# Kernel optimization log

Hardware: AMD Instinct MI355X
Metric: run time of the kernel (lower is better)

The kernel has to match this reference:

```python
import jax, jax.numpy as jnp
import numpy as np

N, T = 32, 1024
CIN, H, O, F2 = 64, 128, 16, 16  # F2 = 2 * FiLMed_layers
EPS = 1e-5
SLOPE = 0.01  # nn.LeakyReLU default


def _leaky(x):
    return jnp.where(x >= 0, x, SLOPE * x)


def _ln(x, gamma, beta):
    # x: (N,T,O,H); gamma,beta: (O,H) -> broadcast per channel
    mu = jnp.mean(x, axis=-1, keepdims=True)
    var = jnp.mean(jnp.square(x - mu), axis=-1, keepdims=True)
    return (x - mu) * jax.lax.rsqrt(var + EPS) * gamma + beta


def setup_inputs() -> dict:
    key = jax.random.key(0)
    ks = jax.random.split(key, 7)
    s0 = 1.0 / np.sqrt(CIN)
    s1 = 1.0 / np.sqrt(H)
    return {
        "x": jax.random.normal(ks[0], (N, T, CIN), jnp.float32),
        "W0": jax.random.uniform(ks[1], (O, H, CIN), jnp.float32, -s0, s0),
        "b0": jax.random.uniform(ks[2], (O, H), jnp.float32, -s0, s0),
        "g0": jnp.ones((O, H), jnp.float32),
        "be0": jnp.zeros((O, H), jnp.float32),
        "W1": jax.random.uniform(ks[3], (O, H, H), jnp.float32, -s1, s1),
        "b1": jax.random.uniform(ks[4], (O, H), jnp.float32, -s1, s1),
        "g1": jnp.ones((O, H), jnp.float32),
        "be1": jnp.zeros((O, H), jnp.float32),
        "W2": jax.random.uniform(ks[5], (O, F2, H), jnp.float32, -s1, s1),
        "b2": jax.random.uniform(ks[6], (O, F2), jnp.float32, -s1, s1),
    }


def reference(x, W0, b0, g0, be0, W1, b1, g1, be1, W2, b2):
    # Per-channel MLP, vectorized over the O channel axis.
    h = jnp.einsum("ntc,ohc->ntoh", x, W0) + b0          # (N,T,O,H)
    h = _ln(_leaky(h), g0, be0)
    h = jnp.einsum("ntoh,ogh->ntog", h, W1) + b1         # (N,T,O,H)
    h = _ln(_leaky(h), g1, be1)
    out = jnp.einsum("ntoh,ofh->ntof", h, W2) + b2       # (N,T,O,F2)
    out = _leaky(out)
    # torch: stack(dim=1) -> (N,O,T,F2); moveaxis(1,-1) -> (N,T,F2,O)
    return jnp.moveaxis(out, 2, 3)
```

## Files before the change

### kernel.cpp

```cpp
#include <hip/hip_runtime.h>
#include <hip/hip_bf16.h>

#define NTOK  32768
#define CIN   64
#define HDIM  128
#define O_CH  16
#define F2    16
#define SLOPE 0.01f
#define EPS   1e-5f

#define SW0_STRIDE 72
#define SW1_STRIDE 136
#define SW2_STRIDE 136
#define SH_STRIDE  136
#define SW0_OFF 0
#define SW1_OFF 9216
#define SW2_OFF (9216 + 17408)
#define WIMG_SHORTS 28800
#define SH_OFF  28800
#define SH_ROWS 256
#define SBIAS_OFF (SH_OFF + SH_ROWS * SH_STRIDE)
#define SBIAS_FLOATS 272
#define SGB_OFF (SBIAS_OFF + SBIAS_FLOATS * 2)
#define SGB_FLOATS 512
#define SMEM_SHORTS (SGB_OFF + SGB_FLOATS * 2)

typedef __attribute__((ext_vector_type(8))) short bf16x8;
typedef __attribute__((ext_vector_type(4))) short bf16x4;
typedef __attribute__((ext_vector_type(4))) float f32x4;

__device__ __forceinline__ unsigned short f2b(float f) {
  union { float f; unsigned int i; } v;
  v.f = f;
  unsigned int i = v.i;
  unsigned int r = (i + 0x7fffu + ((i >> 16) & 1u)) >> 16;
  return (unsigned short)r;
}
__device__ __forceinline__ short f2bn(float f) {
  union { __hip_bfloat16 h; short s; } v;
  v.h = __float2bfloat16(f);
  return v.s;
}
__device__ __forceinline__ float leaky(float t) {
  return fmaxf(t, SLOPE * t);
}
__device__ __forceinline__ bf16x8 cvt8(const float* __restrict__ p) {
  float4 a = *(const float4*)p;
  float4 b = *(const float4*)(p + 4);
  bf16x8 r;
  r[0] = (short)f2b(a.x); r[1] = (short)f2b(a.y);
  r[2] = (short)f2b(a.z); r[3] = (short)f2b(a.w);
  r[4] = (short)f2b(b.x); r[5] = (short)f2b(b.y);
  r[6] = (short)f2b(b.z); r[7] = (short)f2b(b.w);
  return r;
}
__device__ __forceinline__ bf16x8 cvt8s(const float* __restrict__ p,
                                        const float* __restrict__ s) {
  bf16x8 r;
#pragma unroll
  for (int i = 0; i < 8; ++i) r[i] = (short)f2b(p[i] * s[i]);
  return r;
}

__device__ __forceinline__ void leaky_ln_store(
    f32x4* acc, unsigned short* __restrict__ sh,
    int row0, int lo16, int quad) {
  float a0 = 0.f, a1 = 0.f, a2 = 0.f, a3 = 0.f;
  float c0 = 0.f, c1 = 0.f, c2 = 0.f, c3 = 0.f;
#pragma unroll
  for (int nt = 0; nt < 8; ++nt) {
    float t0 = leaky(acc[nt][0]);
    float t1 = leaky(acc[nt][1]);
    float t2 = leaky(acc[nt][2]);
    float t3 = leaky(acc[nt][3]);
    acc[nt][0] = t0; acc[nt][1] = t1; acc[nt][2] = t2; acc[nt][3] = t3;
    a0 += t0; a1 += t1; a2 += t2; a3 += t3;
    c0 = fmaf(t0, t0, c0); c1 = fmaf(t1, t1, c1);
    c2 = fmaf(t2, t2, c2); c3 = fmaf(t3, t3, c3);
  }
  float s1 = (a0 + a1) + (a2 + a3);
  float s2 = (c0 + c1) + (c2 + c3);
  s1 += __shfl_xor(s1, 16); s2 += __shfl_xor(s2, 16);
  s1 += __shfl_xor(s1, 32); s2 += __shfl_xor(s2, 32);
  float mu = s1 * (1.0f / 128.0f);
  float var = s2 * (1.0f / 128.0f) - mu * mu;
  float rs = rsqrtf(var + EPS);
  float nm = -mu * rs;
  unsigned short* dst = sh + (row0 + lo16) * SH_STRIDE + quad * 4;
#pragma unroll
  for (int nt = 0; nt < 8; ++nt) {
    bf16x4 p;
    p[0] = f2bn(fmaf(acc[nt][0], rs, nm));
    p[1] = f2bn(fmaf(acc[nt][1], rs, nm));
    p[2] = f2bn(fmaf(acc[nt][2], rs, nm));
    p[3] = f2bn(fmaf(acc[nt][3], rs, nm));
    *(bf16x4*)(dst + nt * 16) = p;
  }
}

__global__ __launch_bounds__(1024)
__attribute__((amdgpu_waves_per_eu(4, 4))) void film_main(
    const float* __restrict__ x,
    const float* __restrict__ W0, const float* __restrict__ b0,
    const float* __restrict__ g0, const float* __restrict__ be0,
    const float* __restrict__ W1, const float* __restrict__ b1,
    const float* __restrict__ g1, const float* __restrict__ be1,
    const float* __restrict__ W2, const float* __restrict__ b2,
    float* __restrict__ out) {
  __shared__ unsigned short smem[SMEM_SHORTS];
  const int tid = threadIdx.x;
  const int c   = blockIdx.x & 7;
  const int o   = (blockIdx.x >> 3) & 15;
  const int q   = blockIdx.x >> 7;
  const int tok0 = (q * 8 + c) * 1024;

  float* sbias = (float*)&smem[SBIAS_OFF];
  float* sgb   = (float*)&smem[SGB_OFF];
  float* sg0v  = sgb;
  float* sbe0v = sgb + 128;
  float* sg1v  = sgb + 256;
  float* sbe1v = sgb + 384;

  if (tid < 128)      sg0v [tid]       = g0 [o * HDIM + tid];
  else if (tid < 256) sbe0v[tid - 128] = be0[o * HDIM + (tid - 128)];
  else if (tid < 384) sg1v [tid - 256] = g1 [o * HDIM + (tid - 256)];
  else if (tid < 512) sbe1v[tid - 384] = be1[o * HDIM + (tid - 384)];
  __syncthreads();

  const float* w0 = W0 + (size_t)o * HDIM * CIN;
  const float* w1 = W1 + (size_t)o * HDIM * HDIM;
  const float* w2 = W2 + (size_t)o * F2 * HDIM;
  {
    int cc = tid, n = cc >> 3, k8 = cc & 7;
    *(bf16x8*)&smem[SW0_OFF + n * SW0_STRIDE + k8 * 8] = cvt8(w0 + cc * 8);
  }
#pragma unroll
  for (int rep = 0; rep < 2; ++rep) {
    int cc = tid + rep * 1024, n = cc >> 4, k8 = cc & 15;
    *(bf16x8*)&smem[SW1_OFF + n * SW1_STRIDE + k8 * 8] =
        cvt8s(w1 + cc * 8, sg0v + k8 * 8);
  }
  if (tid < 256) {
    int cc = tid, n = cc >> 4, k8 = cc & 15;
    *(bf16x8*)&smem[SW2_OFF + n * SW2_STRIDE + k8 * 8] =
        cvt8s(w2 + cc * 8, sg1v + k8 * 8);
  }
  if (tid < 128) sbias[tid] = b0[o * HDIM + tid];
  {
    int h = tid >> 3, seg = tid & 7;
    const float* w1r = w1 + (size_t)h * HDIM + seg * 16;
    const float* bev = sbe0v + seg * 16;
    float p = 0.f;
#pragma unroll
    for (int k = 0; k < 16; ++k) p = fmaf(w1r[k], bev[k], p);
    p += __shfl_xor(p, 1); p += __shfl_xor(p, 2); p += __shfl_xor(p, 4);
    if (seg == 0) sbias[HDIM + h] = b1[o * HDIM + h] + p;
  }
  if (tid < 128) {
    int f = tid >> 3, seg = tid & 7;
    const float* w2r = w2 + (size_t)f * HDIM + seg * 16;
    const float* bev = sbe1v + seg * 16;
    float p = 0.f;
#pragma unroll
    for (int k = 0; k < 16; ++k) p = fmaf(w2r[k], bev[k], p);
    p += __shfl_xor(p, 1); p += __shfl_xor(p, 2); p += __shfl_xor(p, 4);
    if (seg == 0) sbias[2 * HDIM + f] = b2[o * F2 + f] + p;
  }

  const int lane = tid & 63;
  const int wave = tid >> 6;
  const int lo16 = lane & 15;
  const int quad = lane >> 4;
  const int row0 = wave * 16;
  const float* sb0 = sbias;
  const float* sb1 = sbias + HDIM;
  const float* sb2 = sbias + 2 * HDIM;

  const int tbase = tok0 + wave * 64;
  const float* xw = x + (size_t)(tbase + lo16) * CIN + quad * 8;
  float4 xa0 = *(const float4*)(xw);
  float4 xb0 = *(const float4*)(xw + 4);
  float4 xa1 = *(const float4*)(xw + 32);
  float4 xb1 = *(const float4*)(xw + 36);
  __syncthreads();

  for (int mt = 0; mt < 4; ++mt) {
    const int trow = tbase + mt * 16;

    bf16x8 bx0, bx1;
    bx0[0] = f2bn(xa0.x); bx0[1] = f2bn(xa0.y);
    bx0[2] = f2bn(xa0.z); bx0[3] = f2bn(xa0.w);
    bx0[4] = f2bn(xb0.x); bx0[5] = f2bn(xb0.y);
    bx0[6] = f2bn(xb0.z); bx0[7] = f2bn(xb0.w);
    bx1[0] = f2bn(xa1.x); bx1[1] = f2bn(xa1.y);
    bx1[2] = f2bn(xa1.z); bx1[3] = f2bn(xa1.w);
    bx1[4] = f2bn(xb1.x); bx1[5] = f2bn(xb1.y);
    bx1[6] = f2bn(xb1.z); bx1[7] = f2bn(xb1.w);
    if (mt < 3) {
      const float* xn = xw + (size_t)(mt + 1) * 16 * CIN;
      xa0 = *(const float4*)(xn);
      xb0 = *(const float4*)(xn + 4);
      xa1 = *(const float4*)(xn + 32);
      xb1 = *(const float4*)(xn + 36);
    }

    f32x4 acc[8];
#pragma unroll
    for (int nt = 0; nt < 8; ++nt)
      acc[nt] = *(const f32x4*)(sb0 + nt * 16 + quad * 4);
#pragma unroll
    for (int nt = 0; nt < 8; ++nt) {
      bf16x8 a = *(const bf16x8*)
          &smem[SW0_OFF + (nt * 16 + lo16) * SW0_STRIDE + quad * 8];
      acc[nt] = __builtin_amdgcn_mfma_f32_16x16x32_bf16(a, bx0, acc[nt], 0, 0, 0);
    }
#pragma unroll
    for (int nt = 0; nt < 8; ++nt) {
      bf16x8 a = *(const bf16x8*)
          &smem[SW0_OFF + (nt * 16 + lo16) * SW0_STRIDE + 32 + quad * 8];
      acc[nt] = __builtin_amdgcn_mfma_f32_16x16x32_bf16(a, bx1, acc[nt], 0, 0, 0);
    }
    leaky_ln_store(acc, smem + SH_OFF, row0, lo16, quad);

#pragma unroll
    for (int nt = 0; nt < 8; ++nt)
      acc[nt] = *(const f32x4*)(sb1 + nt * 16 + quad * 4);
#pragma unroll
    for (int ks = 0; ks < 4; ++ks) {
      bf16x8 bh = *(const bf16x8*)
          &smem[SH_OFF + (row0 + lo16) * SH_STRIDE + ks * 32 + quad * 8];
#pragma unroll
      for (int nt = 0; nt < 8; ++nt) {
        bf16x8 a = *(const bf16x8*)
            &smem[SW1_OFF + (nt * 16 + lo16) * SW1_STRIDE + ks * 32 + quad * 8];
        acc[nt] = __builtin_amdgcn_mfma_f32_16x16x32_bf16(a, bh, acc[nt], 0, 0, 0);
      }
    }
    leaky_ln_store(acc, smem + SH_OFF, row0, lo16, quad);

    f32x4 acc2 = *(const f32x4*)(sb2 + quad * 4);
#pragma unroll
    for (int ks = 0; ks < 4; ++ks) {
      bf16x8 bh = *(const bf16x8*)
          &smem[SH_OFF + (row0 + lo16) * SH_STRIDE + ks * 32 + quad * 8];
      bf16x8 a = *(const bf16x8*)
          &smem[SW2_OFF + lo16 * SW2_STRIDE + ks * 32 + quad * 8];
      acc2 = __builtin_amdgcn_mfma_f32_16x16x32_bf16(a, bh, acc2, 0, 0, 0);
    }
    {
      const size_t tb = (size_t)(trow + lo16) * (F2 * O_CH);
#pragma unroll
      for (int r = 0; r < 4; ++r)
        out[tb + (quad * 4 + r) * O_CH + o] = leaky(acc2[r]);
    }
  }
}

extern "C" void kernel_launch(void* const* d_in, const int* in_sizes, int n_in,
                              void* d_out, int out_size, void* d_ws, size_t ws_size,
                              hipStream_t stream) {
  (void)in_sizes; (void)n_in; (void)out_size; (void)d_ws; (void)ws_size;
  const float* x   = (const float*)d_in[0];
  const float* W0  = (const float*)d_in[1];
  const float* b0  = (const float*)d_in[2];
  const float* g0  = (const float*)d_in[3];
  const float* be0 = (const float*)d_in[4];
  const float* W1  = (const float*)d_in[5];
  const float* b1  = (const float*)d_in[6];
  const float* g1  = (const float*)d_in[7];
  const float* be1 = (const float*)d_in[8];
  const float* W2  = (const float*)d_in[9];
  const float* b2  = (const float*)d_in[10];

  film_main<<<dim3(O_CH * (NTOK / 1024)), dim3(1024), 0, stream>>>(
      x, W0, b0, g0, be0, W1, b1, g1, be1, W2, b2, (float*)d_out);
}
```

Baseline: 146.6 us.

## Double tokens per block and pack LeakyReLU/LayerNorm math into float2 vectors

Each block now processes 2048 tokens (eight 16-row tiles per wave) instead of 1024, which halves the grid to 256 blocks and spreads the per-block weight staging and bias folding over twice as many tokens. The LeakyReLU plus LayerNorm epilogue is rewritten with two-wide float vectors so the compiler can emit packed FP32 instructions. The trade-off is fewer blocks to balance across CUs, and the block index decode (c, o, q) is unchanged, so coverage with the smaller grid depends on that mapping still being correct.

```diff
diff --git a/kernel.cpp b/kernel.cpp
--- a/kernel.cpp
+++ b/kernel.cpp
@@ -6,6 +6,7 @@
 #define HDIM  128
 #define O_CH  16
 #define F2    16
+#define MT    8
 #define SLOPE 0.01f
 #define EPS   1e-5f
 
@@ -28,6 +29,7 @@
 typedef __attribute__((ext_vector_type(8))) short bf16x8;
 typedef __attribute__((ext_vector_type(4))) short bf16x4;
 typedef __attribute__((ext_vector_type(4))) float f32x4;
+typedef __attribute__((ext_vector_type(2))) float f32x2;
 
 __device__ __forceinline__ unsigned short f2b(float f) {
   union { float f; unsigned int i; } v;
@@ -43,6 +45,19 @@
 }
 __device__ __forceinline__ float leaky(float t) {
   return fmaxf(t, SLOPE * t);
+}
+__device__ __forceinline__ f32x2 leaky2(f32x2 t) {
+#if __has_builtin(__builtin_elementwise_max) && __has_builtin(__builtin_elementwise_min)
+  f32x2 z = {0.f, 0.f};
+  f32x2 pos = __builtin_elementwise_max(t, z);
+  f32x2 neg = __builtin_elementwise_min(t, z);
+  return pos + SLOPE * neg;
+#else
+  f32x2 r;
+  r.x = fmaxf(t.x, SLOPE * t.x);
+  r.y = fmaxf(t.y, SLOPE * t.y);
+  return r;
+#endif
 }
 __device__ __forceinline__ bf16x8 cvt8(const float* __restrict__ p) {
   float4 a = *(const float4*)p;
@@ -65,35 +80,39 @@
 __device__ __forceinline__ void leaky_ln_store(
     f32x4* acc, unsigned short* __restrict__ sh,
     int row0, int lo16, int quad) {
-  float a0 = 0.f, a1 = 0.f, a2 = 0.f, a3 = 0.f;
-  float c0 = 0.f, c1 = 0.f, c2 = 0.f, c3 = 0.f;
+  f32x2 sa = {0.f, 0.f}, sb = {0.f, 0.f};
+  f32x2 qa = {0.f, 0.f}, qb = {0.f, 0.f};
 #pragma unroll
   for (int nt = 0; nt < 8; ++nt) {
-    float t0 = leaky(acc[nt][0]);
-    float t1 = leaky(acc[nt][1]);
-    float t2 = leaky(acc[nt][2]);
-    float t3 = leaky(acc[nt][3]);
-    acc[nt][0] = t0; acc[nt][1] = t1; acc[nt][2] = t2; acc[nt][3] = t3;
-    a0 += t0; a1 += t1; a2 += t2; a3 += t3;
-    c0 = fmaf(t0, t0, c0); c1 = fmaf(t1, t1, c1);
-    c2 = fmaf(t2, t2, c2); c3 = fmaf(t3, t3, c3);
-  }
-  float s1 = (a0 + a1) + (a2 + a3);
-  float s2 = (c0 + c1) + (c2 + c3);
+    f32x2 u0 = {acc[nt][0], acc[nt][1]};
+    f32x2 u1 = {acc[nt][2], acc[nt][3]};
+    u0 = leaky2(u0);
+    u1 = leaky2(u1);
+    acc[nt][0] = u0.x; acc[nt][1] = u0.y;
+    acc[nt][2] = u1.x; acc[nt][3] = u1.y;
+    sa += u0; sb += u1;
+    qa += u0 * u0;
+    qb += u1 * u1;
+  }
+  float s1 = (sa.x + sa.y) + (sb.x + sb.y);
+  float s2 = (qa.x + qa.y) + (qb.x + qb.y);
   s1 += __shfl_xor(s1, 16); s2 += __shfl_xor(s2, 16);
   s1 += __shfl_xor(s1, 32); s2 += __shfl_xor(s2, 32);
   float mu = s1 * (1.0f / 128.0f);
   float var = s2 * (1.0f / 128.0f) - mu * mu;
   float rs = rsqrtf(var + EPS);
   float nm = -mu * rs;
+  const f32x2 rs2 = {rs, rs}, nm2 = {nm, nm};
   unsigned short* dst = sh + (row0 + lo16) * SH_STRIDE + quad * 4;
 #pragma unroll
   for (int nt = 0; nt < 8; ++nt) {
+    f32x2 u0 = {acc[nt][0], acc[nt][1]};
+    f32x2 u1 = {acc[nt][2], acc[nt][3]};
+    u0 = u0 * rs2 + nm2;
+    u1 = u1 * rs2 + nm2;
     bf16x4 p;
-    p[0] = f2bn(fmaf(acc[nt][0], rs, nm));
-    p[1] = f2bn(fmaf(acc[nt][1], rs, nm));
-    p[2] = f2bn(fmaf(acc[nt][2], rs, nm));
-    p[3] = f2bn(fmaf(acc[nt][3], rs, nm));
+    p[0] = f2bn(u0.x); p[1] = f2bn(u0.y);
+    p[2] = f2bn(u1.x); p[3] = f2bn(u1.y);
     *(bf16x4*)(dst + nt * 16) = p;
   }
 }
@@ -112,7 +131,7 @@
   const int c   = blockIdx.x & 7;
   const int o   = (blockIdx.x >> 3) & 15;
   const int q   = blockIdx.x >> 7;
-  const int tok0 = (q * 8 + c) * 1024;
+  const int tok0 = (q * 8 + c) * (16 * 16 * MT);
 
   float* sbias = (float*)&smem[SBIAS_OFF];
   float* sgb   = (float*)&smem[SGB_OFF];
@@ -176,7 +195,7 @@
   const float* sb1 = sbias + HDIM;
   const float* sb2 = sbias + 2 * HDIM;
 
-  const int tbase = tok0 + wave * 64;
+  const int tbase = tok0 + wave * (16 * MT);
   const float* xw = x + (size_t)(tbase + lo16) * CIN + quad * 8;
   float4 xa0 = *(const float4*)(xw);
   float4 xb0 = *(const float4*)(xw + 4);
@@ -184,7 +203,7 @@
   float4 xb1 = *(const float4*)(xw + 36);
   __syncthreads();
 
-  for (int mt = 0; mt < 4; ++mt) {
+  for (int mt = 0; mt < MT; ++mt) {
     const int trow = tbase + mt * 16;
 
     bf16x8 bx0, bx1;
@@ -196,7 +215,7 @@
     bx1[2] = f2bn(xa1.z); bx1[3] = f2bn(xa1.w);
     bx1[4] = f2bn(xb1.x); bx1[5] = f2bn(xb1.y);
     bx1[6] = f2bn(xb1.z); bx1[7] = f2bn(xb1.w);
-    if (mt < 3) {
+    if (mt < MT - 1) {
       const float* xn = xw + (size_t)(mt + 1) * 16 * CIN;
       xa0 = *(const float4*)(xn);
       xb0 = *(const float4*)(xn + 4);
@@ -272,6 +291,6 @@
   const float* W2  = (const float*)d_in[9];
   const float* b2  = (const float*)d_in[10];
 
-  film_main<<<dim3(O_CH * (NTOK / 1024)), dim3(1024), 0, stream>>>(
+  film_main<<<dim3(O_CH * (NTOK / (16 * 16 * MT))), dim3(1024), 0, stream>>>(
       x, W0, b0, g0, be0, W1, b1, g1, be1, W2, b2, (float*)d_out);
 }
```

Measured after the change: 141.4 us. -3.6%, faster.
